# Kernel optimization log

Hardware: AMD Instinct MI355X
Metric: run time of the kernel (lower is better)

Reference implementation:

```python
import jax, jax.numpy as jnp
import numpy as np

DIM = 2048
HQ = 32
HKV = 8
HD = DIM // HQ  # 64
B, T = 2, 2048


def _rope_tables(key_unused):
    # Standard RoPE tables: cos/sin of shape [B, T, HD]
    inv_freq = 1.0 / (10000.0 ** (np.arange(0, HD, 2, dtype=np.float32) / HD))
    t = np.arange(T, dtype=np.float32)
    freqs = np.outer(t, inv_freq)                 # [T, HD/2]
    emb = np.concatenate([freqs, freqs], axis=-1)  # [T, HD]
    cos = jnp.asarray(np.cos(emb))[None].repeat(B, axis=0)
    sin = jnp.asarray(np.sin(emb))[None].repeat(B, axis=0)
    return cos, sin


def setup_inputs() -> dict:
    key = jax.random.key(0)
    ks = jax.random.split(key, 8)
    s_in = 1.0 / np.sqrt(DIM)
    x = jax.random.normal(ks[0], (B, T, DIM), dtype=jnp.float32)
    cos, sin = _rope_tables(None)
    # Linear weights stored as [in, out] (transposed vs torch)
    Wq = jax.random.normal(ks[1], (DIM, HQ * HD), dtype=jnp.float32) * s_in
    bq = jnp.zeros((HQ * HD,), dtype=jnp.float32)
    Wk = jax.random.normal(ks[2], (DIM, HKV * HD), dtype=jnp.float32) * s_in
    bk = jnp.zeros((HKV * HD,), dtype=jnp.float32)
    Wv = jax.random.normal(ks[3], (DIM, HKV * HD), dtype=jnp.float32) * s_in
    bv = jnp.zeros((HKV * HD,), dtype=jnp.float32)
    Wo = jax.random.normal(ks[4], (HQ * HD, DIM), dtype=jnp.float32) * s_in
    return {"x": x, "cos": cos, "sin": sin, "Wq": Wq, "bq": bq,
            "Wk": Wk, "bk": bk, "Wv": Wv, "bv": bv, "Wo": Wo}


def _rotate_half(u):
    u1, u2 = jnp.split(u, 2, axis=-1)
    return jnp.concatenate([-u2, u1], axis=-1)


def reference(x, cos, sin, Wq, bq, Wk, bk, Wv, bv, Wo):
    Bx, Tx, D = x.shape
    g = HQ // HKV  # group size (queries per kv head)
    q = (x @ Wq + bq).reshape(Bx, Tx, HQ, HD).transpose(0, 2, 1, 3)   # [B,Hq,T,d]
    k = (x @ Wk + bk).reshape(Bx, Tx, HKV, HD).transpose(0, 2, 1, 3)  # [B,Hkv,T,d]
    v = (x @ Wv + bv).reshape(Bx, Tx, HKV, HD).transpose(0, 2, 1, 3)
    c = cos[:, None, :, :]  # [B,1,T,d]
    s = sin[:, None, :, :]
    q = q * c + _rotate_half(q) * s
    k = k * c + _rotate_half(k) * s
    # GQA: group query heads over shared KV heads instead of repeat_interleave
    qg = q.reshape(Bx, HKV, g, Tx, HD)
    scale = 1.0 / np.sqrt(HD)
    scores = jnp.einsum('bkgtd,bksd->bkgts', qg, k) * scale  # [B,Hkv,g,T,T]
    causal = jnp.tril(jnp.ones((Tx, Tx), dtype=bool))
    scores = jnp.where(causal, scores, jnp.finfo(scores.dtype).min)
    probs = jax.nn.softmax(scores, axis=-1)
    out = jnp.einsum('bkgts,bksd->bkgtd', probs, v)           # [B,Hkv,g,T,d]
    out = out.reshape(Bx, HQ, Tx, HD).transpose(0, 2, 1, 3).reshape(Bx, Tx, HQ * HD)
    return out @ Wo
```

## Files before the change

kernel.cpp:

```cpp
#include <hip/hip_runtime.h>


typedef short s8v __attribute__((ext_vector_type(8)));
typedef float f4v __attribute__((ext_vector_type(4)));

__device__ __forceinline__ unsigned short f2bf(float f) {
  unsigned int u = __float_as_uint(f);
  u += 0x7fffu + ((u >> 16) & 1u);
  return (unsigned short)(u >> 16);
}

__device__ __forceinline__ unsigned int pk_bf16(float a, float b) {
#if __has_builtin(__builtin_amdgcn_cvt_pk_bf16_f32)
  auto r = __builtin_amdgcn_cvt_pk_bf16_f32(a, b);
  return *(unsigned int*)&r;
#else
  return (unsigned int)f2bf(a) | ((unsigned int)f2bf(b) << 16);
#endif
}

__device__ __forceinline__ void llds16(const void* g, void* l) {
  __builtin_amdgcn_global_load_lds(
      (__attribute__((address_space(1))) void*)(g),
      (__attribute__((address_space(3))) void*)(l), 16, 0, 0);
}

__global__ __launch_bounds__(256) void prep_k(const float* __restrict__ x,
    const float* __restrict__ Wq, const float* __restrict__ Wk,
    const float* __restrict__ Wv, const float* __restrict__ Wo,
    unsigned short* __restrict__ xb, unsigned short* __restrict__ Wt,
    unsigned short* __restrict__ Wot) {
  const int tid = threadIdx.x;
  int bid = blockIdx.x;
  if (bid < 8192) {
    const int i = bid * 256 + tid;
    float4 v = ((const float4*)x)[i];
    ushort4 o;
    o.x = f2bf(v.x); o.y = f2bf(v.y); o.z = f2bf(v.z); o.w = f2bf(v.w);
    ((ushort4*)xb)[i] = o;
    return;
  }
  bid -= 8192;
  const float* src; unsigned short* dst; int srcW, bx, by;
  if (bid < 4096)      { src = Wq; dst = Wt;                        srcW = 2048; bx = bid & 63;        by = bid >> 6; }
  else if (bid < 5120) { src = Wk; dst = Wt + (size_t)2048 * 2048;  srcW = 512;  bx = (bid - 4096) & 15; by = (bid - 4096) >> 4; }
  else if (bid < 6144) { src = Wv; dst = Wt + (size_t)2560 * 2048;  srcW = 512;  bx = (bid - 5120) & 15; by = (bid - 5120) >> 4; }
  else                 { src = Wo; dst = Wot;                       srcW = 2048; bx = (bid - 6144) & 63; by = (bid - 6144) >> 6; }
  __shared__ float tile[32][33];
  const int tx = tid & 31, ty = tid >> 5;
  const int xg = bx * 32 + tx;
  const int ybase = by * 32;
#pragma unroll
  for (int j = 0; j < 32; j += 8)
    tile[ty + j][tx] = src[(size_t)(ybase + ty + j) * srcW + xg];
  __syncthreads();
  const int x2 = ybase + tx;
  const int y2 = bx * 32 + ty;
#pragma unroll
  for (int j = 0; j < 32; j += 8)
    dst[(size_t)(y2 + j) * 2048 + x2] = f2bf(tile[tx][ty + j]);
}

__device__ __forceinline__ void gemm128_db(const unsigned short* __restrict__ A,
                                           const unsigned short* __restrict__ Bt,
                                           int K, int m0, int n0,
                                           unsigned short (*As)[4096],
                                           unsigned short (*Bs)[4096],
                                           f4v acc[4][4]) {
  const int tid = threadIdx.x;
  const int lane = tid & 63;
  const int w = tid >> 6;
  const int wm = w >> 1, wn = w & 1;
  const int c = lane & 15, quad = lane >> 4;
  const int srow = tid >> 2;
  const int scol = ((tid & 3) ^ ((tid >> 3) & 3)) * 8;
  const int ca = (quad ^ ((c >> 1) & 3)) * 8;
  const unsigned short* ga0 = A + (size_t)(m0 + srow) * K + scol;
  const unsigned short* gb0 = Bt + (size_t)(n0 + srow) * K + scol;

  llds16(ga0,          As[0] + w * 512);
  llds16(ga0 + 64 * K, As[0] + 2048 + w * 512);
  llds16(gb0,          Bs[0] + w * 512);
  llds16(gb0 + 64 * K, Bs[0] + 2048 + w * 512);
  __syncthreads();

  const int niter = K >> 5;
  for (int it = 0; it < niter; ++it) {
    const int cur = it & 1;
    if (it + 1 < niter) {
      const int kk = (it + 1) << 5, nxt = cur ^ 1;
      llds16(ga0 + kk,          As[nxt] + w * 512);
      llds16(ga0 + kk + 64 * K, As[nxt] + 2048 + w * 512);
      llds16(gb0 + kk,          Bs[nxt] + w * 512);
      llds16(gb0 + kk + 64 * K, Bs[nxt] + 2048 + w * 512);
    }
    s8v a[4], b[4];
#pragma unroll
    for (int i = 0; i < 4; ++i)
      a[i] = *(const s8v*)&As[cur][(wm * 64 + i * 16 + c) * 32 + ca];
#pragma unroll
    for (int i = 0; i < 4; ++i)
      b[i] = *(const s8v*)&Bs[cur][(wn * 64 + i * 16 + c) * 32 + ca];
#pragma unroll
    for (int mb = 0; mb < 4; ++mb)
#pragma unroll
      for (int nb = 0; nb < 4; ++nb)
        acc[mb][nb] = __builtin_amdgcn_mfma_f32_16x16x32_bf16(a[mb], b[nb], acc[mb][nb], 0, 0, 0);
    __syncthreads();
  }
}

__global__ __launch_bounds__(256) void gemm_qkv(const unsigned short* __restrict__ A,
    const unsigned short* __restrict__ Bt,
    const float* __restrict__ bq, const float* __restrict__ bk, const float* __restrict__ bv,
    const float* __restrict__ cosp, const float* __restrict__ sinp,
    unsigned short* __restrict__ Qb, unsigned short* __restrict__ Kb,
    unsigned short* __restrict__ Vt) {
  __shared__ unsigned short As[2][4096], Bs[2][4096];
  const f4v fzero = {0.f, 0.f, 0.f, 0.f};
  f4v acc[4][4];
#pragma unroll
  for (int i = 0; i < 4; ++i)
#pragma unroll
    for (int j = 0; j < 4; ++j) acc[i][j] = fzero;
  const int m0 = blockIdx.y * 128, n0 = blockIdx.x * 128;
  gemm128_db(A, Bt, 2048, m0, n0, As, Bs, acc);

  const int tid = threadIdx.x, lane = tid & 63, w = tid >> 6;
  const int wm = w >> 1, wn = w & 1, c = lane & 15, quad = lane >> 4;
  const int nbase = n0 + wn * 64;
  const float QSC = 0.125f * 1.44269504089f;
#pragma unroll
  for (int mb = 0; mb < 4; ++mb) {
#pragma unroll
    for (int r = 0; r < 4; ++r) {
      const int row = m0 + wm * 64 + mb * 16 + quad * 4 + r;
      const int b = row >> 11, t = row & 2047;
      if (nbase < 2048) {
        const int h = nbase >> 6;
        const size_t ob = ((size_t)(b * 32 + h) * 2048 + t) * 64;
        const float* cb = cosp + (size_t)row * 64;
        const float* sb = sinp + (size_t)row * 64;
#pragma unroll
        for (int nb = 0; nb < 2; ++nb) {
          const int d0 = nb * 16 + c, d1 = d0 + 32;
          const float v0 = acc[mb][nb][r] + bq[nbase + d0];
          const float v1 = acc[mb][nb + 2][r] + bq[nbase + d1];
          Qb[ob + d0] = f2bf((v0 * cb[d0] - v1 * sb[d0]) * QSC);
          Qb[ob + d1] = f2bf((v1 * cb[d1] + v0 * sb[d1]) * QSC);
        }
      } else if (nbase < 2560) {
        const int h = (nbase - 2048) >> 6;
        const size_t ob = ((size_t)(b * 8 + h) * 2048 + t) * 64;
        const float* cb = cosp + (size_t)row * 64;
        const float* sb = sinp + (size_t)row * 64;
#pragma unroll
        for (int nb = 0; nb < 2; ++nb) {
          const int d0 = nb * 16 + c, d1 = d0 + 32;
          const float v0 = acc[mb][nb][r] + bk[nbase - 2048 + d0];
          const float v1 = acc[mb][nb + 2][r] + bk[nbase - 2048 + d1];
          Kb[ob + d0] = f2bf(v0 * cb[d0] - v1 * sb[d0]);
          Kb[ob + d1] = f2bf(v1 * cb[d1] + v0 * sb[d1]);
        }
      } else {
        const int h = (nbase - 2560) >> 6;
        const size_t vb = (size_t)(b * 8 + h) * 64;
        const int tl = t & 63;
        const int tp = (t & ~63) | (((tl & 15) << 2) | (tl >> 4));
#pragma unroll
        for (int nb = 0; nb < 4; ++nb) {
          const int d = nb * 16 + c;
          Vt[(vb + d) * 2048 + tp] = f2bf(acc[mb][nb][r] + bv[nbase - 2560 + d]);
        }
      }
    }
  }
}

__global__ __launch_bounds__(256) void attn_k(const unsigned short* __restrict__ Qb,
                                              const unsigned short* __restrict__ Kb,
                                              const unsigned short* __restrict__ Vt,
                                              unsigned short* __restrict__ An) {
  __shared__ unsigned short QPs[4096];
  __shared__ unsigned short Ks[2][4096], Vs[2][4096];
  const int tid = threadIdx.x, lane = tid & 63, w = tid >> 6;
  const int c = lane & 15, quad = lane >> 4;
  const int bh = blockIdx.y;
  const int b = bh >> 5, h = bh & 31, kvh = h >> 2;
  const int qt = gridDim.x - 1 - blockIdx.x;
  const int q0 = qt * 64;
  const unsigned short* gQ = Qb + ((size_t)bh * 2048 + q0) * 64;
  const unsigned short* gK = Kb + (size_t)(b * 8 + kvh) * 2048 * 64;
  const unsigned short* gV = Vt + (size_t)(b * 8 + kvh) * 64 * 2048;

  const int r0 = tid >> 3;
  const int ch8 = ((tid & 7) ^ (r0 & 7)) * 8;

  llds16(gQ + r0 * 64 + ch8,        QPs + w * 512);
  llds16(gQ + (r0 + 32) * 64 + ch8, QPs + 2048 + w * 512);
  llds16(gK + r0 * 64 + ch8,        Ks[0] + w * 512);
  llds16(gK + (r0 + 32) * 64 + ch8, Ks[0] + 2048 + w * 512);
  llds16(gV + (size_t)r0 * 2048 + ch8,        Vs[0] + w * 512);
  llds16(gV + (size_t)(r0 + 32) * 2048 + ch8, Vs[0] + 2048 + w * 512);
  __syncthreads();

  const int xq0 = (quad ^ (c & 7)) * 8;
  const int xq1 = ((quad + 4) ^ (c & 7)) * 8;
  const s8v aq0 = *(const s8v*)&QPs[(w * 16 + c) * 64 + xq0];
  const s8v aq1 = *(const s8v*)&QPs[(w * 16 + c) * 64 + xq1];

  const f4v fzero = {0.f, 0.f, 0.f, 0.f};
  f4v O[4];
  float lrp[4];
#pragma unroll
  for (int i = 0; i < 4; ++i) { O[i] = fzero; lrp[i] = 0.f; }

  const int ntiles = qt + 1;
  for (int it = 0; it < ntiles; ++it) {
    const int cur = it & 1;
    if (it + 1 < ntiles) {
      const int s1 = (it + 1) * 64, nxt = cur ^ 1;
      llds16(gK + (size_t)(s1 + r0) * 64 + ch8,      Ks[nxt] + w * 512);
      llds16(gK + (size_t)(s1 + r0 + 32) * 64 + ch8, Ks[nxt] + 2048 + w * 512);
      llds16(gV + (size_t)r0 * 2048 + s1 + ch8,        Vs[nxt] + w * 512);
      llds16(gV + (size_t)(r0 + 32) * 2048 + s1 + ch8, Vs[nxt] + 2048 + w * 512);
    }

    f4v S[4];
#pragma unroll
    for (int nb = 0; nb < 4; ++nb) {
      const s8v bk0 = *(const s8v*)&Ks[cur][(nb * 16 + c) * 64 + xq0];
      const s8v bk1 = *(const s8v*)&Ks[cur][(nb * 16 + c) * 64 + xq1];
      f4v z = fzero;
      z = __builtin_amdgcn_mfma_f32_16x16x32_bf16(aq0, bk0, z, 0, 0, 0);
      z = __builtin_amdgcn_mfma_f32_16x16x32_bf16(aq1, bk1, z, 0, 0, 0);
      S[nb] = z;
    }

    const bool diag = (it == qt);
#pragma unroll
    for (int r = 0; r < 4; ++r) {
      const int rloc = quad * 4 + r;
      float p[4];
#pragma unroll
      for (int nb = 0; nb < 4; ++nb) {
        float sv = S[nb][r];
        if (diag && (nb * 16 + c > w * 16 + rloc)) sv = -1e30f;
        p[nb] = __builtin_amdgcn_exp2f(sv);
      }
      lrp[r] += (p[0] + p[1]) + (p[2] + p[3]);
      uint2 pk2;
      pk2.x = pk_bf16(p[0], p[1]);
      pk2.y = pk_bf16(p[2], p[3]);
      *(uint2*)&QPs[w * 1024 + rloc * 64 + (((c >> 1) ^ (rloc & 7)) * 8) + (c & 1) * 4] = pk2;
    }
    asm volatile("s_waitcnt lgkmcnt(0)" ::: "memory");

    const s8v ap0 = *(const s8v*)&QPs[w * 1024 + c * 64 + xq0];
    const s8v ap1 = *(const s8v*)&QPs[w * 1024 + c * 64 + xq1];
#pragma unroll
    for (int nbd = 0; nbd < 4; ++nbd) {
      const s8v bv0 = *(const s8v*)&Vs[cur][(nbd * 16 + c) * 64 + xq0];
      const s8v bv1 = *(const s8v*)&Vs[cur][(nbd * 16 + c) * 64 + xq1];
      O[nbd] = __builtin_amdgcn_mfma_f32_16x16x32_bf16(ap0, bv0, O[nbd], 0, 0, 0);
      O[nbd] = __builtin_amdgcn_mfma_f32_16x16x32_bf16(ap1, bv1, O[nbd], 0, 0, 0);
    }
    __syncthreads();
  }

#pragma unroll
  for (int r = 0; r < 4; ++r) {
    float ps = lrp[r];
    ps += __shfl_xor(ps, 1, 64);
    ps += __shfl_xor(ps, 2, 64);
    ps += __shfl_xor(ps, 4, 64);
    ps += __shfl_xor(ps, 8, 64);
    const float inv = 1.0f / ps;
    const int t = q0 + w * 16 + quad * 4 + r;
    const size_t rowb = ((size_t)b * 2048 + t) * 2048 + h * 64;
#pragma unroll
    for (int nbd = 0; nbd < 4; ++nbd)
      An[rowb + nbd * 16 + c] = f2bf(O[nbd][r] * inv);
  }
}

__global__ __launch_bounds__(256) void gemm_out(const unsigned short* __restrict__ A,
                                                const unsigned short* __restrict__ Bt,
                                                float* __restrict__ C) {
  __shared__ unsigned short As[2][4096], Bs[2][4096];
  const f4v fzero = {0.f, 0.f, 0.f, 0.f};
  f4v acc[4][4];
#pragma unroll
  for (int i = 0; i < 4; ++i)
#pragma unroll
    for (int j = 0; j < 4; ++j) acc[i][j] = fzero;
  const int m0 = blockIdx.y * 128, n0 = blockIdx.x * 128;
  gemm128_db(A, Bt, 2048, m0, n0, As, Bs, acc);
  const int tid = threadIdx.x, lane = tid & 63, w = tid >> 6;
  const int wm = w >> 1, wn = w & 1, c = lane & 15, quad = lane >> 4;
#pragma unroll
  for (int mb = 0; mb < 4; ++mb)
#pragma unroll
    for (int r = 0; r < 4; ++r) {
      const int row = m0 + wm * 64 + mb * 16 + quad * 4 + r;
#pragma unroll
      for (int nb = 0; nb < 4; ++nb)
        C[(size_t)row * 2048 + n0 + wn * 64 + nb * 16 + c] = acc[mb][nb][r];
    }
}

extern "C" void kernel_launch(void* const* d_in, const int* in_sizes, int n_in,
                              void* d_out, int out_size, void* d_ws, size_t ws_size,
                              hipStream_t stream) {
  const float* x    = (const float*)d_in[0];
  const float* cosp = (const float*)d_in[1];
  const float* sinp = (const float*)d_in[2];
  const float* Wq   = (const float*)d_in[3];
  const float* bq   = (const float*)d_in[4];
  const float* Wk   = (const float*)d_in[5];
  const float* bk   = (const float*)d_in[6];
  const float* Wv   = (const float*)d_in[7];
  const float* bv   = (const float*)d_in[8];
  const float* Wo   = (const float*)d_in[9];
  float* out = (float*)d_out;

  char* ws = (char*)d_ws;
  unsigned short* xb  = (unsigned short*)(ws);
  unsigned short* Wt  = (unsigned short*)(ws + 16777216);
  unsigned short* Wot = (unsigned short*)(ws + 29360128);
  unsigned short* Qb  = (unsigned short*)(ws + 37748736);
  unsigned short* Kb  = (unsigned short*)(ws + 54525952);
  unsigned short* Vt  = (unsigned short*)(ws + 58720256);
  unsigned short* An  = (unsigned short*)(ws + 62914560);

  prep_k<<<18432, 256, 0, stream>>>(x, Wq, Wk, Wv, Wo, xb, Wt, Wot);
  gemm_qkv<<<dim3(24, 32), 256, 0, stream>>>(xb, Wt, bq, bk, bv, cosp, sinp, Qb, Kb, Vt);
  attn_k<<<dim3(32, 64), 256, 0, stream>>>(Qb, Kb, Vt, An);
  gemm_out<<<dim3(16, 32), 256, 0, stream>>>(An, Wot, out);
}
```

Baseline: 365.7 us.

## Process 128 query rows per attention block to reuse K/V tiles

Each attention workgroup now handles two 64-row query sub-tiles (128 rows) instead of one, so every K/V tile loaded into LDS feeds twice as many MFMAs and global K/V traffic is halved. The grid shrinks from 32 to 16 query tiles per head, and causal masking is applied separately to each sub-tile's diagonal. In exchange, LDS and register use per block rise and there are half as many blocks, which can lower occupancy and make the causal workload less evenly balanced.

```diff
diff --git a/kernel.cpp b/kernel.cpp
--- a/kernel.cpp
+++ b/kernel.cpp
@@ -181,14 +181,14 @@
                                               const unsigned short* __restrict__ Kb,
                                               const unsigned short* __restrict__ Vt,
                                               unsigned short* __restrict__ An) {
-  __shared__ unsigned short QPs[4096];
+  __shared__ unsigned short QPs[8192];
   __shared__ unsigned short Ks[2][4096], Vs[2][4096];
   const int tid = threadIdx.x, lane = tid & 63, w = tid >> 6;
   const int c = lane & 15, quad = lane >> 4;
   const int bh = blockIdx.y;
   const int b = bh >> 5, h = bh & 31, kvh = h >> 2;
   const int qt = gridDim.x - 1 - blockIdx.x;
-  const int q0 = qt * 64;
+  const int q0 = qt * 128;
   const unsigned short* gQ = Qb + ((size_t)bh * 2048 + q0) * 64;
   const unsigned short* gK = Kb + (size_t)(b * 8 + kvh) * 2048 * 64;
   const unsigned short* gV = Vt + (size_t)(b * 8 + kvh) * 64 * 2048;
@@ -196,8 +196,10 @@
   const int r0 = tid >> 3;
   const int ch8 = ((tid & 7) ^ (r0 & 7)) * 8;
 
-  llds16(gQ + r0 * 64 + ch8,        QPs + w * 512);
-  llds16(gQ + (r0 + 32) * 64 + ch8, QPs + 2048 + w * 512);
+  llds16(gQ + r0 * 64 + ch8,         QPs + w * 512);
+  llds16(gQ + (r0 + 32) * 64 + ch8,  QPs + 2048 + w * 512);
+  llds16(gQ + (r0 + 64) * 64 + ch8,  QPs + 4096 + w * 512);
+  llds16(gQ + (r0 + 96) * 64 + ch8,  QPs + 6144 + w * 512);
   llds16(gK + r0 * 64 + ch8,        Ks[0] + w * 512);
   llds16(gK + (r0 + 32) * 64 + ch8, Ks[0] + 2048 + w * 512);
   llds16(gV + (size_t)r0 * 2048 + ch8,        Vs[0] + w * 512);
@@ -206,16 +208,24 @@
 
   const int xq0 = (quad ^ (c & 7)) * 8;
   const int xq1 = ((quad + 4) ^ (c & 7)) * 8;
-  const s8v aq0 = *(const s8v*)&QPs[(w * 16 + c) * 64 + xq0];
-  const s8v aq1 = *(const s8v*)&QPs[(w * 16 + c) * 64 + xq1];
+  s8v aq[2][2];
+#pragma unroll
+  for (int j = 0; j < 2; ++j) {
+    aq[j][0] = *(const s8v*)&QPs[(j * 64 + w * 16 + c) * 64 + xq0];
+    aq[j][1] = *(const s8v*)&QPs[(j * 64 + w * 16 + c) * 64 + xq1];
+  }
 
   const f4v fzero = {0.f, 0.f, 0.f, 0.f};
-  f4v O[4];
-  float lrp[4];
-#pragma unroll
-  for (int i = 0; i < 4; ++i) { O[i] = fzero; lrp[i] = 0.f; }
-
-  const int ntiles = qt + 1;
+  f4v O[2][4];
+  float lrp[2][4];
+#pragma unroll
+  for (int j = 0; j < 2; ++j)
+#pragma unroll
+    for (int i = 0; i < 4; ++i) { O[j][i] = fzero; lrp[j][i] = 0.f; }
+
+  const int pbase0 = w * 1024, pbase1 = 4096 + w * 1024;
+
+  const int ntiles = 2 * qt + 2;
   for (int it = 0; it < ntiles; ++it) {
     const int cur = it & 1;
     if (it + 1 < ntiles) {
@@ -226,62 +236,93 @@
       llds16(gV + (size_t)(r0 + 32) * 2048 + s1 + ch8, Vs[nxt] + 2048 + w * 512);
     }
 
-    f4v S[4];
+    const bool rb0v = (it <= 2 * qt);
+    const bool diag0 = (it == 2 * qt);
+    const bool diag1 = (it == 2 * qt + 1);
+
+    f4v S0[4], S1[4];
 #pragma unroll
     for (int nb = 0; nb < 4; ++nb) {
       const s8v bk0 = *(const s8v*)&Ks[cur][(nb * 16 + c) * 64 + xq0];
       const s8v bk1 = *(const s8v*)&Ks[cur][(nb * 16 + c) * 64 + xq1];
+      if (rb0v) {
+        f4v z = fzero;
+        z = __builtin_amdgcn_mfma_f32_16x16x32_bf16(aq[0][0], bk0, z, 0, 0, 0);
+        z = __builtin_amdgcn_mfma_f32_16x16x32_bf16(aq[0][1], bk1, z, 0, 0, 0);
+        S0[nb] = z;
+      }
       f4v z = fzero;
-      z = __builtin_amdgcn_mfma_f32_16x16x32_bf16(aq0, bk0, z, 0, 0, 0);
-      z = __builtin_amdgcn_mfma_f32_16x16x32_bf16(aq1, bk1, z, 0, 0, 0);
-      S[nb] = z;
-    }
-
-    const bool diag = (it == qt);
+      z = __builtin_amdgcn_mfma_f32_16x16x32_bf16(aq[1][0], bk0, z, 0, 0, 0);
+      z = __builtin_amdgcn_mfma_f32_16x16x32_bf16(aq[1][1], bk1, z, 0, 0, 0);
+      S1[nb] = z;
+    }
+
+    if (rb0v) {
+#pragma unroll
+      for (int r = 0; r < 4; ++r) {
+        const int rloc = quad * 4 + r;
+        float p[4];
+#pragma unroll
+        for (int nb = 0; nb < 4; ++nb) {
+          float sv = S0[nb][r];
+          if (diag0 && (nb * 16 + c > w * 16 + rloc)) sv = -1e30f;
+          p[nb] = __builtin_amdgcn_exp2f(sv);
+        }
+        lrp[0][r] += (p[0] + p[1]) + (p[2] + p[3]);
+        uint2 pk2; pk2.x = pk_bf16(p[0], p[1]); pk2.y = pk_bf16(p[2], p[3]);
+        *(uint2*)&QPs[pbase0 + rloc * 64 + (((c >> 1) ^ (rloc & 7)) * 8) + (c & 1) * 4] = pk2;
+      }
+    }
 #pragma unroll
     for (int r = 0; r < 4; ++r) {
       const int rloc = quad * 4 + r;
       float p[4];
 #pragma unroll
       for (int nb = 0; nb < 4; ++nb) {
-        float sv = S[nb][r];
-        if (diag && (nb * 16 + c > w * 16 + rloc)) sv = -1e30f;
+        float sv = S1[nb][r];
+        if (diag1 && (nb * 16 + c > w * 16 + rloc)) sv = -1e30f;
         p[nb] = __builtin_amdgcn_exp2f(sv);
       }
-      lrp[r] += (p[0] + p[1]) + (p[2] + p[3]);
-      uint2 pk2;
-      pk2.x = pk_bf16(p[0], p[1]);
-      pk2.y = pk_bf16(p[2], p[3]);
-      *(uint2*)&QPs[w * 1024 + rloc * 64 + (((c >> 1) ^ (rloc & 7)) * 8) + (c & 1) * 4] = pk2;
+      lrp[1][r] += (p[0] + p[1]) + (p[2] + p[3]);
+      uint2 pk2; pk2.x = pk_bf16(p[0], p[1]); pk2.y = pk_bf16(p[2], p[3]);
+      *(uint2*)&QPs[pbase1 + rloc * 64 + (((c >> 1) ^ (rloc & 7)) * 8) + (c & 1) * 4] = pk2;
     }
     asm volatile("s_waitcnt lgkmcnt(0)" ::: "memory");
 
-    const s8v ap0 = *(const s8v*)&QPs[w * 1024 + c * 64 + xq0];
-    const s8v ap1 = *(const s8v*)&QPs[w * 1024 + c * 64 + xq1];
+    const s8v ap00 = *(const s8v*)&QPs[pbase0 + c * 64 + xq0];
+    const s8v ap01 = *(const s8v*)&QPs[pbase0 + c * 64 + xq1];
+    const s8v ap10 = *(const s8v*)&QPs[pbase1 + c * 64 + xq0];
+    const s8v ap11 = *(const s8v*)&QPs[pbase1 + c * 64 + xq1];
 #pragma unroll
     for (int nbd = 0; nbd < 4; ++nbd) {
       const s8v bv0 = *(const s8v*)&Vs[cur][(nbd * 16 + c) * 64 + xq0];
       const s8v bv1 = *(const s8v*)&Vs[cur][(nbd * 16 + c) * 64 + xq1];
-      O[nbd] = __builtin_amdgcn_mfma_f32_16x16x32_bf16(ap0, bv0, O[nbd], 0, 0, 0);
-      O[nbd] = __builtin_amdgcn_mfma_f32_16x16x32_bf16(ap1, bv1, O[nbd], 0, 0, 0);
+      if (rb0v) {
+        O[0][nbd] = __builtin_amdgcn_mfma_f32_16x16x32_bf16(ap00, bv0, O[0][nbd], 0, 0, 0);
+        O[0][nbd] = __builtin_amdgcn_mfma_f32_16x16x32_bf16(ap01, bv1, O[0][nbd], 0, 0, 0);
+      }
+      O[1][nbd] = __builtin_amdgcn_mfma_f32_16x16x32_bf16(ap10, bv0, O[1][nbd], 0, 0, 0);
+      O[1][nbd] = __builtin_amdgcn_mfma_f32_16x16x32_bf16(ap11, bv1, O[1][nbd], 0, 0, 0);
     }
     __syncthreads();
   }
 
 #pragma unroll
-  for (int r = 0; r < 4; ++r) {
-    float ps = lrp[r];
-    ps += __shfl_xor(ps, 1, 64);
-    ps += __shfl_xor(ps, 2, 64);
-    ps += __shfl_xor(ps, 4, 64);
-    ps += __shfl_xor(ps, 8, 64);
-    const float inv = 1.0f / ps;
-    const int t = q0 + w * 16 + quad * 4 + r;
-    const size_t rowb = ((size_t)b * 2048 + t) * 2048 + h * 64;
-#pragma unroll
-    for (int nbd = 0; nbd < 4; ++nbd)
-      An[rowb + nbd * 16 + c] = f2bf(O[nbd][r] * inv);
-  }
+  for (int j = 0; j < 2; ++j)
+#pragma unroll
+    for (int r = 0; r < 4; ++r) {
+      float ps = lrp[j][r];
+      ps += __shfl_xor(ps, 1, 64);
+      ps += __shfl_xor(ps, 2, 64);
+      ps += __shfl_xor(ps, 4, 64);
+      ps += __shfl_xor(ps, 8, 64);
+      const float inv = 1.0f / ps;
+      const int t = q0 + j * 64 + w * 16 + quad * 4 + r;
+      const size_t rowb = ((size_t)b * 2048 + t) * 2048 + h * 64;
+#pragma unroll
+      for (int nbd = 0; nbd < 4; ++nbd)
+        An[rowb + nbd * 16 + c] = f2bf(O[j][nbd][r] * inv);
+    }
 }
 
 __global__ __launch_bounds__(256) void gemm_out(const unsigned short* __restrict__ A,
@@ -335,6 +376,6 @@
 
   prep_k<<<18432, 256, 0, stream>>>(x, Wq, Wk, Wv, Wo, xb, Wt, Wot);
   gemm_qkv<<<dim3(24, 32), 256, 0, stream>>>(xb, Wt, bq, bk, bv, cosp, sinp, Qb, Kb, Vt);
-  attn_k<<<dim3(32, 64), 256, 0, stream>>>(Qb, Kb, Vt, An);
+  attn_k<<<dim3(16, 64), 256, 0, stream>>>(Qb, Kb, Vt, An);
   gemm_out<<<dim3(16, 32), 256, 0, stream>>>(An, Wot, out);
 }
```

After: 376.5 us. 2.9% more time.
